# Kernel tuning notes

Hardware: AMD Instinct MI355X
Metric: run time of the kernel (lower is better)

## Reference

```python
import jax, jax.numpy as jnp
import numpy as np

B, SW, SE, D, H, FF = 8, 512, 128, 1024, 16, 4096
HD = D // H
EPS = 1e-12
SCALE = 1.0 / np.sqrt(HD).astype(np.float32)


def _split_heads(x):
    # [B, S, D] -> [B, H, S, HD]
    b, s, _ = x.shape
    return x.reshape(b, s, H, HD).transpose(0, 2, 1, 3)


def _layer_norm(x, g, b):
    m = jnp.mean(x, axis=-1, keepdims=True)
    v = jnp.mean(jnp.square(x - m), axis=-1, keepdims=True)
    return g * (x - m) / jnp.sqrt(v + EPS) + b


def setup_inputs() -> dict:
    key = jax.random.key(0)
    ks = iter(jax.random.split(key, 40))
    std = 0.02

    def w(i, o):
        return jax.random.normal(next(ks), (i, o), jnp.float32) * std

    inp = {
        "word_hidden_states": jax.random.normal(next(ks), (B, SW, D), jnp.float32),
        "entity_hidden_states": jax.random.normal(next(ks), (B, SE, D), jnp.float32),
        "word_attention_mask": jnp.zeros((B, SW), jnp.float32),
        "entity_attention_mask": jnp.zeros((B, SE), jnp.float32),
        # entity-aware self attention projections
        "Wq": w(D, D), "bq": jnp.zeros((D,), jnp.float32),
        "Ww2e": w(D, D), "bw2e": jnp.zeros((D,), jnp.float32),
        "We2w": w(D, D), "be2w": jnp.zeros((D,), jnp.float32),
        "We2e": w(D, D), "be2e": jnp.zeros((D,), jnp.float32),
        "Wk": w(D, D), "bk": jnp.zeros((D,), jnp.float32),
        "Wv": w(D, D), "bv": jnp.zeros((D,), jnp.float32),
        # BertSelfOutput
        "Wo": w(D, D), "bo": jnp.zeros((D,), jnp.float32),
        "ln1_g": jnp.ones((D,), jnp.float32), "ln1_b": jnp.zeros((D,), jnp.float32),
        # BertIntermediate / BertOutput
        "Wi": w(D, FF), "bi": jnp.zeros((FF,), jnp.float32),
        "Wout": w(FF, D), "bout": jnp.zeros((D,), jnp.float32),
        "ln2_g": jnp.ones((D,), jnp.float32), "ln2_b": jnp.zeros((D,), jnp.float32),
    }
    return inp


def _layer(wh, eh, wmask, emask, Wq, bq, Ww2e, bw2e, We2w, be2w, We2e, be2e,
           Wk, bk, Wv, bv, Wo, bo, ln1_g, ln1_b, Wi, bi, Wout, bout, ln2_g, ln2_b):
    sw = wh.shape[1]
    hidden = jnp.concatenate([wh, eh], axis=1)              # [B, S, D]
    mask = jnp.concatenate([wmask, emask], axis=-1)[:, None, None, :]  # additive

    q_w2w = _split_heads(wh @ Wq + bq)
    q_w2e = _split_heads(wh @ Ww2e + bw2e)
    q_e2w = _split_heads(eh @ We2w + be2w)
    q_e2e = _split_heads(eh @ We2e + be2e)
    k = _split_heads(hidden @ Wk + bk)                      # [B, H, S, HD]
    kw, ke = k[:, :, :sw, :], k[:, :, sw:, :]

    s_w2w = jnp.einsum("bhqd,bhkd->bhqk", q_w2w, kw)
    s_w2e = jnp.einsum("bhqd,bhkd->bhqk", q_w2e, ke)
    s_e2w = jnp.einsum("bhqd,bhkd->bhqk", q_e2w, kw)
    s_e2e = jnp.einsum("bhqd,bhkd->bhqk", q_e2e, ke)
    word_scores = jnp.concatenate([s_w2w, s_w2e], axis=3)
    ent_scores = jnp.concatenate([s_e2w, s_e2e], axis=3)
    scores = jnp.concatenate([word_scores, ent_scores], axis=2) * SCALE + mask
    probs = jax.nn.softmax(scores, axis=-1)

    v = _split_heads(hidden @ Wv + bv)
    ctx = jnp.einsum("bhqk,bhkd->bhqd", probs, v)
    ctx = ctx.transpose(0, 2, 1, 3).reshape(wh.shape[0], -1, D)  # [B, S, D]

    # BertSelfOutput: dense + residual + LN
    attn_out = _layer_norm(ctx @ Wo + bo + hidden, ln1_g, ln1_b)
    # BertIntermediate + BertOutput
    inter = jax.nn.gelu(attn_out @ Wi + bi, approximate=False)
    out = _layer_norm(inter @ Wout + bout + attn_out, ln2_g, ln2_b)
    return out[:, :sw, :], out[:, sw:, :]


def reference(word_hidden_states, entity_hidden_states, word_attention_mask,
              entity_attention_mask, Wq, bq, Ww2e, bw2e, We2w, be2w, We2e, be2e,
              Wk, bk, Wv, bv, Wo, bo, ln1_g, ln1_b, Wi, bi, Wout, bout,
              ln2_g, ln2_b):
    return _layer(word_hidden_states, entity_hidden_states, word_attention_mask,
                  entity_attention_mask, Wq, bq, Ww2e, bw2e, We2w, be2w, We2e,
                  be2e, Wk, bk, Wv, bv, Wo, bo, ln1_g, ln1_b, Wi, bi, Wout,
                  bout, ln2_g, ln2_b)
```

## Files before the change

kernel.cpp:

```cpp
#include <hip/hip_runtime.h>
#include <hip/hip_bf16.h>
#include <stdint.h>
#include <math.h>

#define DEV __device__ __forceinline__

using bf16 = __hip_bfloat16;
typedef __attribute__((ext_vector_type(8))) short bf16x8;
typedef __attribute__((ext_vector_type(4))) float f32x4;

static constexpr int NB  = 8;
static constexpr int NSW = 512;
static constexpr int NSE = 128;
static constexpr int ND  = 1024;
static constexpr int NH  = 16;
static constexpr int NFF = 4096;
static constexpr int NS  = NSW + NSE;
static constexpr int NHD = 64;

DEV f32x4 mfma16(bf16x8 a, bf16x8 b, f32x4 c){
  return __builtin_amdgcn_mfma_f32_16x16x32_bf16(a, b, c, 0, 0, 0);
}

DEV void gload16(const bf16* g, bf16* l){
  __builtin_amdgcn_global_load_lds((const __attribute__((address_space(1))) void*)g,
                                   (__attribute__((address_space(3))) void*)l,
                                   16, 0, 0);
}

DEV bf16 tobf(float f){ return __float2bfloat16(f); }

union PK4 { bf16 h[4]; short4 s; };

__global__ __launch_bounds__(256) void cast_word_k(const float* __restrict__ wh,
                                                   bf16* __restrict__ whb,
                                                   bf16* __restrict__ hid){
  long i = ((long)blockIdx.x*256 + threadIdx.x)*4;
  float4 v = *reinterpret_cast<const float4*>(wh + i);
  PK4 p; p.h[0]=tobf(v.x); p.h[1]=tobf(v.y); p.h[2]=tobf(v.z); p.h[3]=tobf(v.w);
  *reinterpret_cast<short4*>(whb + i) = p.s;
  long row = i >> 10; int c = (int)(i & 1023);
  int b = (int)(row >> 9), s = (int)(row & 511);
  *reinterpret_cast<short4*>(hid + ((long)(b*NS + s) << 10) + c) = p.s;
}

__global__ __launch_bounds__(256) void cast_ent_k(const float* __restrict__ eh,
                                                  bf16* __restrict__ ehb,
                                                  bf16* __restrict__ hid){
  long i = ((long)blockIdx.x*256 + threadIdx.x)*4;
  float4 v = *reinterpret_cast<const float4*>(eh + i);
  PK4 p; p.h[0]=tobf(v.x); p.h[1]=tobf(v.y); p.h[2]=tobf(v.z); p.h[3]=tobf(v.w);
  *reinterpret_cast<short4*>(ehb + i) = p.s;
  long row = i >> 10; int c = (int)(i & 1023);
  int b = (int)(row >> 7), s = (int)(row & 127);
  *reinterpret_cast<short4*>(hid + ((long)(b*NS + NSW + s) << 10) + c) = p.s;
}

struct TP7 { const float* src[7]; bf16* dst[7]; };

__global__ void transpose7_k(TP7 tp){
  __shared__ float tile[32][33];
  const float* in = tp.src[blockIdx.z];
  bf16* out = tp.dst[blockIdx.z];
  const int c0 = blockIdx.x*32, r0 = blockIdx.y*32;
  const int tx = threadIdx.x, ty = threadIdx.y;
  #pragma unroll
  for (int i=0;i<4;i++)
    tile[ty + i*8][tx] = in[(long)(r0 + ty + i*8)*1024 + c0 + tx];
  __syncthreads();
  #pragma unroll
  for (int i=0;i<4;i++){
    int rr = ty + i*8;
    out[(long)(c0 + rr)*1024 + r0 + tx] = tobf(tile[tx][rr]);
  }
}

__global__ void transpose_cast_k(const float* __restrict__ in, bf16* __restrict__ out,
                                 int R, int C){
  __shared__ float tile[32][33];
  const int c0 = blockIdx.x*32, r0 = blockIdx.y*32;
  const int tx = threadIdx.x, ty = threadIdx.y;
  #pragma unroll
  for (int i=0;i<4;i++)
    tile[ty + i*8][tx] = in[(long)(r0 + ty + i*8)*C + c0 + tx];
  __syncthreads();
  #pragma unroll
  for (int i=0;i<4;i++){
    int rr = ty + i*8;
    out[(long)(c0 + rr)*R + r0 + tx] = tobf(tile[tx][rr]);
  }
}

__global__ void bias_concat_k(const float* __restrict__ bq, const float* __restrict__ bw2e,
                              const float* __restrict__ be2w, const float* __restrict__ be2e,
                              const float* __restrict__ bk, const float* __restrict__ bv,
                              float* __restrict__ bQw, float* __restrict__ bQe,
                              float* __restrict__ bKV){
  int i = blockIdx.x*256 + threadIdx.x;
  bQw[i] = bq[i];   bQw[1024+i] = bw2e[i];
  bQe[i] = be2w[i]; bQe[1024+i] = be2e[i];
  bKV[i] = bk[i];   bKV[1024+i] = bv[i];
}

template<int EPI>
__global__ __launch_bounds__(256) void gemm_bt_k(const bf16* __restrict__ A,
                                                 const bf16* __restrict__ Bt,
                                                 const float* __restrict__ bias,
                                                 void* __restrict__ Cout,
                                                 void* __restrict__ Cout2,
                                                 int M, int N, int K){
  __shared__ __align__(16) bf16 As[128*64];
  __shared__ __align__(16) bf16 Bs[128*64];
  const int tid = threadIdx.x;

  const int nwg = gridDim.x*gridDim.y;
  const int orig = blockIdx.y*gridDim.x + blockIdx.x;
  const int qq = nwg >> 3, rr8 = nwg & 7;
  const int xcd = orig & 7, idx = orig >> 3;
  const int wg = (xcd < rr8 ? xcd*(qq+1) : rr8*(qq+1) + (xcd-rr8)*qq) + idx;
  const int m0 = (wg / gridDim.x)*128, n0 = (wg % gridDim.x)*128;

  const int Kc  = K / gridDim.z;
  const int kt0 = blockIdx.z * Kc;

  const int wid = tid>>6, lane = tid&63;
  const int wr = wid>>1, wc = wid&1;
  const int lr = lane&15, lg = lane>>4;

  const f32x4 zero = {0.f,0.f,0.f,0.f};
  f32x4 acc[4][4];
  #pragma unroll
  for (int m=0;m<4;m++)
    #pragma unroll
    for (int n=0;n<4;n++) acc[m][n] = zero;

  for (int kt=kt0; kt<kt0+Kc; kt+=64){
    #pragma unroll
    for (int i=0;i<4;i++){
      int idx2 = i*256 + tid;
      int row = idx2>>3, kc = idx2&7;
      gload16(A + (long)(m0+row)*K + kt + kc*8, As + idx2*8);
    }
    #pragma unroll
    for (int i=0;i<4;i++){
      int idx2 = i*256 + tid;
      int row = idx2>>3, kc = idx2&7;
      gload16(Bt + (long)(n0+row)*K + kt + kc*8, Bs + idx2*8);
    }
    __syncthreads();
    #pragma unroll
    for (int ks=0; ks<2; ks++){
      bf16x8 af[4], bg[4];
      #pragma unroll
      for (int m=0;m<4;m++)
        af[m] = *reinterpret_cast<const bf16x8*>(As + (wr*64 + m*16 + lr)*64 + ks*32 + lg*8);
      #pragma unroll
      for (int n=0;n<4;n++)
        bg[n] = *reinterpret_cast<const bf16x8*>(Bs + (wc*64 + n*16 + lr)*64 + ks*32 + lg*8);
      __builtin_amdgcn_s_setprio(1);
      #pragma unroll
      for (int m=0;m<4;m++)
        #pragma unroll
        for (int n=0;n<4;n++)
          acc[m][n] = mfma16(af[m], bg[n], acc[m][n]);
      __builtin_amdgcn_s_setprio(0);
    }
    __syncthreads();
  }

  #pragma unroll
  for (int m=0;m<4;m++){
    const int rbase = m0 + wr*64 + m*16 + lg*4;
    #pragma unroll
    for (int n=0;n<4;n++){
      const int col = n0 + wc*64 + n*16 + lr;
      const float bsv = (EPI == 5 && blockIdx.z != 0) ? 0.f : bias[col];
      #pragma unroll
      for (int r=0;r<4;r++){
        const int rw = rbase + r;
        float v = acc[m][n][r] + bsv;
        if constexpr (EPI == 0){
          ((bf16*)Cout)[(long)rw*N + col] = tobf(v);
        } else if constexpr (EPI == 3){
          float ge = 0.5f*v*(1.0f + erff(v*0.70710678118654752f));
          ((bf16*)Cout)[(long)rw*N + col] = tobf(ge);
        } else if constexpr (EPI == 4){
          if (col < 1024){
            ((bf16*)Cout)[(long)rw*2048 + col] = tobf(v);
          } else {
            int bb = rw / NS, ss = rw % NS, hh = (col-1024) >> 6, dd = (col-1024) & 63;
            ((bf16*)Cout2)[((long)((bb*NH + hh)*NHD + dd))*NS + ss] = tobf(v);
          }
        } else {
          float* dst = blockIdx.z == 0 ? (float*)Cout : (float*)Cout2;
          dst[(long)rw*N + col] = v;
        }
      }
    }
  }
}

__global__ __launch_bounds__(256) void attn_k(
    const bf16* __restrict__ Qw,
    const bf16* __restrict__ Qe,
    const bf16* __restrict__ KV,
    const bf16* __restrict__ Vt,
    const float* __restrict__ wm, const float* __restrict__ em,
    bf16* __restrict__ ctx){
  __shared__ __align__(16) bf16 Plds[4][2][16*40];
  __shared__ float mred[4][2][16];
  __shared__ float lred[4][2][16];
  __shared__ __align__(16) float accred[4][16][64];
  const int tid = threadIdx.x, wid = tid>>6, lane = tid&63;
  const int lr = lane&15, lg = lane>>4;
  const int w   = blockIdx.x;
  const int b   = w / (NH*20);
  const int rem = w % (NH*20);
  const int h   = rem / 20;
  const int q0  = (rem % 20)*32;

  const bf16* Qbase; long qrow0;
  if (q0 < NSW){ Qbase = Qw; qrow0 = (long)b*NSW + q0; }
  else         { Qbase = Qe; qrow0 = (long)b*NSE + (q0 - NSW); }

  bf16x8 qA[2][2], qB[2][2];
  #pragma unroll
  for (int m=0;m<2;m++)
    #pragma unroll
    for (int dc=0; dc<2; dc++){
      long o = (qrow0 + m*16 + lr)*2048 + h*NHD + dc*32 + lg*8;
      qA[m][dc] = *reinterpret_cast<const bf16x8*>(Qbase + o);
      qB[m][dc] = *reinterpret_cast<const bf16x8*>(Qbase + o + 1024);
    }

  const f32x4 zero = {0.f,0.f,0.f,0.f};
  f32x4 cacc[2][4];
  float mrow[2][4], lsum[2][4];
  #pragma unroll
  for (int m=0;m<2;m++){
    #pragma unroll
    for (int dt=0;dt<4;dt++) cacc[m][dt] = zero;
    #pragma unroll
    for (int r=0;r<4;r++){ mrow[m][r] = -1e30f; lsum[m][r] = 0.f; }
  }

  const bf16* Kbase = KV + (long)b*NS*2048 + h*NHD;
  const bf16* Vbase = Vt + (long)((b*NH + h)*NHD)*NS;

  for (int kt=wid*5; kt<wid*5+5; kt++){
    const int k0 = kt*32;
    const bool word = (k0 < NSW);

    bf16x8 kf[2][2], vf[4];
    #pragma unroll
    for (int sub=0;sub<2;sub++)
      #pragma unroll
      for (int dc=0;dc<2;dc++)
        kf[sub][dc] = *reinterpret_cast<const bf16x8*>(
            Kbase + (long)(k0 + sub*16 + lr)*2048 + dc*32 + lg*8);
    #pragma unroll
    for (int dt=0;dt<4;dt++)
      vf[dt] = *reinterpret_cast<const bf16x8*>(
          Vbase + (long)(dt*16 + lr)*NS + k0 + lg*8);

    float msk0, msk1;
    { int k = k0 + lr;
      msk0 = word ? wm[b*NSW + k]      : em[b*NSE + (k - NSW)];
      msk1 = word ? wm[b*NSW + k + 16] : em[b*NSE + (k + 16 - NSW)];
    }

    f32x4 sc[2][2];
    #pragma unroll
    for (int m=0;m<2;m++){ sc[m][0]=zero; sc[m][1]=zero; }
    __builtin_amdgcn_s_setprio(1);
    #pragma unroll
    for (int m=0;m<2;m++)
      #pragma unroll
      for (int sub=0;sub<2;sub++)
        #pragma unroll
        for (int dc=0;dc<2;dc++){
          const bf16x8 q = word ? qA[m][dc] : qB[m][dc];
          sc[m][sub] = mfma16(q, kf[sub][dc], sc[m][sub]);
        }
    __builtin_amdgcn_s_setprio(0);

    #pragma unroll
    for (int m=0;m<2;m++){
      bf16* pw = &Plds[wid][m][0];
      #pragma unroll
      for (int r=0;r<4;r++){
        float s0 = sc[m][0][r]*0.125f + msk0;
        float s1 = sc[m][1][r]*0.125f + msk1;
        float t = fmaxf(s0, s1);
        #pragma unroll
        for (int o=8;o;o>>=1) t = fmaxf(t, __shfl_xor(t, o, 16));
        float mn = fmaxf(mrow[m][r], t);
        float al = __expf(mrow[m][r] - mn);
        mrow[m][r] = mn;
        float p0 = __expf(s0 - mn), p1 = __expf(s1 - mn);
        float ps = p0 + p1;
        #pragma unroll
        for (int o=8;o;o>>=1) ps += __shfl_xor(ps, o, 16);
        lsum[m][r] = lsum[m][r]*al + ps;
        pw[(lg*4+r)*40 + lr]      = tobf(p0);
        pw[(lg*4+r)*40 + 16 + lr] = tobf(p1);
        #pragma unroll
        for (int dt=0;dt<4;dt++) cacc[m][dt][r] *= al;
      }
    }

    __builtin_amdgcn_s_setprio(1);
    #pragma unroll
    for (int m=0;m<2;m++){
      bf16x8 pa = *reinterpret_cast<const bf16x8*>(&Plds[wid][m][0] + lr*40 + lg*8);
      #pragma unroll
      for (int dt=0;dt<4;dt++)
        cacc[m][dt] = mfma16(pa, vf[dt], cacc[m][dt]);
    }
    __builtin_amdgcn_s_setprio(0);
  }

  #pragma unroll
  for (int m=0;m<2;m++)
    #pragma unroll
    for (int r=0;r<4;r++)
      if (lr == 0){
        mred[wid][m][lg*4+r] = mrow[m][r];
        lred[wid][m][lg*4+r] = lsum[m][r];
      }
  __syncthreads();

  float Lg[2][4], scl[2][4];
  #pragma unroll
  for (int m=0;m<2;m++)
    #pragma unroll
    for (int r=0;r<4;r++){
      const int row = lg*4 + r;
      float M0 = fmaxf(fmaxf(mred[0][m][row], mred[1][m][row]),
                       fmaxf(mred[2][m][row], mred[3][m][row]));
      float lt = 0.f;
      #pragma unroll
      for (int ww=0; ww<4; ww++)
        lt += lred[ww][m][row] * __expf(mred[ww][m][row] - M0);
      Lg[m][r]  = lt;
      scl[m][r] = __expf(mrow[m][r] - M0);
    }

  const long crow = (long)b*NS + q0;
  #pragma unroll
  for (int m=0;m<2;m++){
    #pragma unroll
    for (int dt=0;dt<4;dt++)
      #pragma unroll
      for (int r=0;r<4;r++)
        accred[wid][dt*4+r][lane] = cacc[m][dt][r] * scl[m][r];
    __syncthreads();
    { const int dt = wid;
      #pragma unroll
      for (int r=0;r<4;r++){
        float s = accred[0][dt*4+r][lane] + accred[1][dt*4+r][lane]
                + accred[2][dt*4+r][lane] + accred[3][dt*4+r][lane];
        s /= Lg[m][r];
        ctx[(crow + m*16 + lg*4 + r)*ND + h*NHD + dt*16 + lr] = tobf(s);
      }
    }
    __syncthreads();
  }
}

DEV void block_red2(float& s1, float& s2){
  __shared__ float red[8];
  #pragma unroll
  for (int o=32;o;o>>=1){ s1 += __shfl_down(s1,o); s2 += __shfl_down(s2,o); }
  int wid = threadIdx.x>>6, lane = threadIdx.x&63;
  if (lane==0){ red[wid]=s1; red[4+wid]=s2; }
  __syncthreads();
  s1 = red[0]+red[1]+red[2]+red[3];
  s2 = red[4]+red[5]+red[6]+red[7];
}

__global__ __launch_bounds__(256) void ln1_k(const float* __restrict__ ctxO,
    const float* __restrict__ ctxO1,
    const float* __restrict__ wh, const float* __restrict__ eh,
    const float* __restrict__ g, const float* __restrict__ be,
    float* __restrict__ outF, bf16* __restrict__ outB){
  const int row = blockIdx.x;
  const int b = row / NS, s = row % NS;
  const float* resid = (s < NSW) ? wh + ((long)(b*NSW + s))*ND
                                 : eh + ((long)(b*NSE + (s-NSW)))*ND;
  const int t = threadIdx.x;
  float4 xv = reinterpret_cast<const float4*>(ctxO + (long)row*ND)[t];
  float4 x1 = reinterpret_cast<const float4*>(ctxO1 + (long)row*ND)[t];
  float4 rv = reinterpret_cast<const float4*>(resid)[t];
  float4 x = make_float4(xv.x+x1.x+rv.x, xv.y+x1.y+rv.y, xv.z+x1.z+rv.z, xv.w+x1.w+rv.w);
  float s1 = x.x+x.y+x.z+x.w;
  float s2 = x.x*x.x + x.y*x.y + x.z*x.z + x.w*x.w;
  block_red2(s1, s2);
  float mean = s1 * (1.f/ND);
  float var  = s2 * (1.f/ND) - mean*mean;
  float rstd = rsqrtf(var + 1e-12f);
  float4 gv = reinterpret_cast<const float4*>(g)[t];
  float4 bv = reinterpret_cast<const float4*>(be)[t];
  float4 y = make_float4(gv.x*(x.x-mean)*rstd + bv.x,
                         gv.y*(x.y-mean)*rstd + bv.y,
                         gv.z*(x.z-mean)*rstd + bv.z,
                         gv.w*(x.w-mean)*rstd + bv.w);
  reinterpret_cast<float4*>(outF + (long)row*ND)[t] = y;
  PK4 p; p.h[0]=tobf(y.x); p.h[1]=tobf(y.y); p.h[2]=tobf(y.z); p.h[3]=tobf(y.w);
  reinterpret_cast<short4*>(outB + (long)row*ND)[t] = p.s;
}

__global__ __launch_bounds__(256) void ln2_k(const float* __restrict__ ffo,
    const float* __restrict__ ffo1,
    const float* __restrict__ attnF, const float* __restrict__ g,
    const float* __restrict__ be, float* __restrict__ out){
  const int row = blockIdx.x;
  const int b = row / NS, s = row % NS;
  const int t = threadIdx.x;
  float4 xv = reinterpret_cast<const float4*>(ffo + (long)row*ND)[t];
  float4 x1 = reinterpret_cast<const float4*>(ffo1 + (long)row*ND)[t];
  float4 rv = reinterpret_cast<const float4*>(attnF + (long)row*ND)[t];
  float4 x = make_float4(xv.x+x1.x+rv.x, xv.y+x1.y+rv.y, xv.z+x1.z+rv.z, xv.w+x1.w+rv.w);
  float s1 = x.x+x.y+x.z+x.w;
  float s2 = x.x*x.x + x.y*x.y + x.z*x.z + x.w*x.w;
  block_red2(s1, s2);
  float mean = s1 * (1.f/ND);
  float var  = s2 * (1.f/ND) - mean*mean;
  float rstd = rsqrtf(var + 1e-12f);
  float4 gv = reinterpret_cast<const float4*>(g)[t];
  float4 bv = reinterpret_cast<const float4*>(be)[t];
  float4 y = make_float4(gv.x*(x.x-mean)*rstd + bv.x,
                         gv.y*(x.y-mean)*rstd + bv.y,
                         gv.z*(x.z-mean)*rstd + bv.z,
                         gv.w*(x.w-mean)*rstd + bv.w);
  float* op = (s < NSW) ? out + ((long)(b*NSW+s))*ND
                        : out + (long)NB*NSW*ND + ((long)(b*NSE + (s-NSW)))*ND;
  reinterpret_cast<float4*>(op)[t] = y;
}

extern "C" void kernel_launch(void* const* d_in, const int* in_sizes, int n_in,
                              void* d_out, int out_size, void* d_ws, size_t ws_size,
                              hipStream_t stream){
  (void)in_sizes; (void)n_in; (void)out_size; (void)ws_size;
  const float* wh   = (const float*)d_in[0];
  const float* eh   = (const float*)d_in[1];
  const float* wm   = (const float*)d_in[2];
  const float* em   = (const float*)d_in[3];
  const float* Wq   = (const float*)d_in[4];   const float* bq   = (const float*)d_in[5];
  const float* Ww2e = (const float*)d_in[6];   const float* bw2e = (const float*)d_in[7];
  const float* We2w = (const float*)d_in[8];   const float* be2w = (const float*)d_in[9];
  const float* We2e = (const float*)d_in[10];  const float* be2e = (const float*)d_in[11];
  const float* Wk   = (const float*)d_in[12];  const float* bk   = (const float*)d_in[13];
  const float* Wv   = (const float*)d_in[14];  const float* bv   = (const float*)d_in[15];
  const float* Wo   = (const float*)d_in[16];  const float* bo   = (const float*)d_in[17];
  const float* g1   = (const float*)d_in[18];  const float* b1   = (const float*)d_in[19];
  const float* Wi   = (const float*)d_in[20];  const float* bi   = (const float*)d_in[21];
  const float* Wout = (const float*)d_in[22];  const float* bout = (const float*)d_in[23];
  const float* g2   = (const float*)d_in[24];  const float* b2   = (const float*)d_in[25];
  float* out = (float*)d_out;

  char* ws = (char*)d_ws;
  size_t off = 0;
  auto alloc = [&](size_t bytes)->char*{
    char* p = ws + off; off += (bytes + 255) & ~(size_t)255; return p;
  };

  bf16* hid   = (bf16*)alloc((size_t)NB*NS*ND*2);
  bf16* whb   = (bf16*)alloc((size_t)NB*NSW*ND*2);
  bf16* ehb   = (bf16*)alloc((size_t)NB*NSE*ND*2);
  float* part1 = (float*)hid;
  bf16* WqwT  = (bf16*)alloc((size_t)2048*ND*2);
  bf16* WqeT  = (bf16*)alloc((size_t)2048*ND*2);
  bf16* WkvT  = (bf16*)alloc((size_t)2048*ND*2);
  bf16* WoT   = (bf16*)alloc((size_t)ND*ND*2);
  bf16* WiT   = (bf16*)alloc((size_t)NFF*ND*2);
  bf16* WoutT = (bf16*)alloc((size_t)ND*NFF*2);
  float* bQw  = (float*)alloc(2048*4);
  float* bQe  = (float*)alloc(2048*4);
  float* bKV  = (float*)alloc(2048*4);

  char* u1 = alloc((size_t)52428800);
  bf16* Qwb = (bf16*)u1;
  bf16* Qeb = Qwb + (size_t)NB*NSW*2048;
  bf16* KVb = Qeb + (size_t)NB*NSE*2048;
  bf16* Vt  = KVb + (size_t)NB*NS*2048;
  bf16* inter = (bf16*)u1;
  bf16* attnB = (bf16*)(u1 + (size_t)41943040);

  bf16*  ctx   = (bf16*)alloc((size_t)NB*NS*ND*2);
  float* ctxO  = (float*)alloc((size_t)NB*NS*ND*4);
  float* ffo   = ctxO;
  float* attnF = (float*)alloc((size_t)NB*NS*ND*4);

  dim3 tb(32,8);
  cast_word_k<<<4096, 256, 0, stream>>>(wh, whb, hid);
  cast_ent_k <<<1024, 256, 0, stream>>>(eh, ehb, hid);

  TP7 tp;
  tp.src[0]=Wq;   tp.dst[0]=WqwT;
  tp.src[1]=Ww2e; tp.dst[1]=WqwT + (size_t)1024*1024;
  tp.src[2]=We2w; tp.dst[2]=WqeT;
  tp.src[3]=We2e; tp.dst[3]=WqeT + (size_t)1024*1024;
  tp.src[4]=Wk;   tp.dst[4]=WkvT;
  tp.src[5]=Wv;   tp.dst[5]=WkvT + (size_t)1024*1024;
  tp.src[6]=Wo;   tp.dst[6]=WoT;
  transpose7_k<<<dim3(32,32,7), tb, 0, stream>>>(tp);
  transpose_cast_k<<<dim3(128,32), tb, 0, stream>>>(Wi,   WiT,   ND, NFF);
  transpose_cast_k<<<dim3(32,128), tb, 0, stream>>>(Wout, WoutT, NFF, ND);
  bias_concat_k<<<4, 256, 0, stream>>>(bq, bw2e, be2w, be2e, bk, bv, bQw, bQe, bKV);

  gemm_bt_k<0><<<dim3(16,32), 256, 0, stream>>>(whb, WqwT, bQw, Qwb, nullptr, NB*NSW, 2048, ND);
  gemm_bt_k<0><<<dim3(16, 8), 256, 0, stream>>>(ehb, WqeT, bQe, Qeb, nullptr, NB*NSE, 2048, ND);
  gemm_bt_k<4><<<dim3(16,40), 256, 0, stream>>>(hid, WkvT, bKV, KVb, Vt,      NB*NS,  2048, ND);

  attn_k<<<2560, 256, 0, stream>>>(Qwb, Qeb, KVb, Vt, wm, em, ctx);

  gemm_bt_k<5><<<dim3(8,40,2),  256, 0, stream>>>(ctx,   WoT,   bo,   ctxO, part1, NB*NS, ND,  ND);
  ln1_k<<<5120, 256, 0, stream>>>(ctxO, part1, wh, eh, g1, b1, attnF, attnB);
  gemm_bt_k<3><<<dim3(32,40),   256, 0, stream>>>(attnB, WiT,   bi,   inter, nullptr, NB*NS, NFF, ND);
  gemm_bt_k<5><<<dim3(8,40,2),  256, 0, stream>>>(inter, WoutT, bout, ffo,  part1, NB*NS, ND,  NFF);
  ln2_k<<<5120, 256, 0, stream>>>(ffo, part1, attnF, g2, b2, out);
}
```

Measured before the change: 563.0 us.

## Replace GEMMs with 256-wide double-buffered core and merge projection launches

Replaces the generic 128x128 single-buffered GEMM with a 512-thread core using 256x256 (or 256x128 for split-K) tiles. The core double-buffers LDS, waits on vmcnt and overlaps the next K-slice loads with MFMA work. Its LDS layout is lane-ordered, so fragment reads are contiguous. The three Q/KV projection GEMMs become one launch that gathers word and entity rows straight from the concatenated hidden buffer, which removes the separate whb/ehb bf16 copies. The aim is to raise data reuse and hide global load latency, at the cost of heavy LDS use that limits occupancy to one block per CU and fewer blocks per launch.

```diff
diff --git a/kernel.cpp b/kernel.cpp
--- a/kernel.cpp
+++ b/kernel.cpp
@@ -33,24 +33,20 @@
 union PK4 { bf16 h[4]; short4 s; };
 
 __global__ __launch_bounds__(256) void cast_word_k(const float* __restrict__ wh,
-                                                   bf16* __restrict__ whb,
                                                    bf16* __restrict__ hid){
   long i = ((long)blockIdx.x*256 + threadIdx.x)*4;
   float4 v = *reinterpret_cast<const float4*>(wh + i);
   PK4 p; p.h[0]=tobf(v.x); p.h[1]=tobf(v.y); p.h[2]=tobf(v.z); p.h[3]=tobf(v.w);
-  *reinterpret_cast<short4*>(whb + i) = p.s;
   long row = i >> 10; int c = (int)(i & 1023);
   int b = (int)(row >> 9), s = (int)(row & 511);
   *reinterpret_cast<short4*>(hid + ((long)(b*NS + s) << 10) + c) = p.s;
 }
 
 __global__ __launch_bounds__(256) void cast_ent_k(const float* __restrict__ eh,
-                                                  bf16* __restrict__ ehb,
                                                   bf16* __restrict__ hid){
   long i = ((long)blockIdx.x*256 + threadIdx.x)*4;
   float4 v = *reinterpret_cast<const float4*>(eh + i);
   PK4 p; p.h[0]=tobf(v.x); p.h[1]=tobf(v.y); p.h[2]=tobf(v.z); p.h[3]=tobf(v.w);
-  *reinterpret_cast<short4*>(ehb + i) = p.s;
   long row = i >> 10; int c = (int)(i & 1023);
   int b = (int)(row >> 7), s = (int)(row & 127);
   *reinterpret_cast<short4*>(hid + ((long)(b*NS + NSW + s) << 10) + c) = p.s;
@@ -102,109 +98,232 @@
   bKV[i] = bk[i];   bKV[1024+i] = bv[i];
 }
 
-template<int EPI>
-__global__ __launch_bounds__(256) void gemm_bt_k(const bf16* __restrict__ A,
-                                                 const bf16* __restrict__ Bt,
-                                                 const float* __restrict__ bias,
-                                                 void* __restrict__ Cout,
-                                                 void* __restrict__ Cout2,
-                                                 int M, int N, int K){
-  __shared__ __align__(16) bf16 As[128*64];
-  __shared__ __align__(16) bf16 Bs[128*64];
-  const int tid = threadIdx.x;
-
-  const int nwg = gridDim.x*gridDim.y;
-  const int orig = blockIdx.y*gridDim.x + blockIdx.x;
-  const int qq = nwg >> 3, rr8 = nwg & 7;
-  const int xcd = orig & 7, idx = orig >> 3;
-  const int wg = (xcd < rr8 ? xcd*(qq+1) : rr8*(qq+1) + (xcd-rr8)*qq) + idx;
-  const int m0 = (wg / gridDim.x)*128, n0 = (wg % gridDim.x)*128;
-
-  const int Kc  = K / gridDim.z;
-  const int kt0 = blockIdx.z * Kc;
-
-  const int wid = tid>>6, lane = tid&63;
-  const int wr = wid>>1, wc = wid&1;
-  const int lr = lane&15, lg = lane>>4;
-
-  const f32x4 zero = {0.f,0.f,0.f,0.f};
-  f32x4 acc[4][4];
-  #pragma unroll
-  for (int m=0;m<4;m++)
-    #pragma unroll
-    for (int n=0;n<4;n++) acc[m][n] = zero;
-
-  for (int kt=kt0; kt<kt0+Kc; kt+=64){
-    #pragma unroll
-    for (int i=0;i<4;i++){
-      int idx2 = i*256 + tid;
-      int row = idx2>>3, kc = idx2&7;
-      gload16(A + (long)(m0+row)*K + kt + kc*8, As + idx2*8);
-    }
-    #pragma unroll
-    for (int i=0;i<4;i++){
-      int idx2 = i*256 + tid;
-      int row = idx2>>3, kc = idx2&7;
-      gload16(Bt + (long)(n0+row)*K + kt + kc*8, Bs + idx2*8);
-    }
-    __syncthreads();
-    #pragma unroll
-    for (int ks=0; ks<2; ks++){
-      bf16x8 af[4], bg[4];
-      #pragma unroll
-      for (int m=0;m<4;m++)
-        af[m] = *reinterpret_cast<const bf16x8*>(As + (wr*64 + m*16 + lr)*64 + ks*32 + lg*8);
-      #pragma unroll
-      for (int n=0;n<4;n++)
-        bg[n] = *reinterpret_cast<const bf16x8*>(Bs + (wc*64 + n*16 + lr)*64 + ks*32 + lg*8);
+template<int NF>
+DEV void stA(bf16* reg, const bf16* a0, const bf16* a1, int koff, int tid){
+  gload16(a0 + koff, reg + tid*8);
+  gload16(a1 + koff, reg + (512 + tid)*8);
+}
+template<int NF>
+DEV void stB(bf16* reg, const bf16* b0, const bf16* b1, int koff, int tid){
+  gload16(b0 + koff, reg + tid*8);
+  if constexpr (NF == 4) gload16(b1 + koff, reg + (512 + tid)*8);
+}
+
+template<int NF>
+DEV void g256_core(const bf16* a0, const bf16* a1,
+                   const bf16* b0, const bf16* b1,
+                   int NT, bf16* lds, f32x4 (&acc)[8][NF],
+                   int tid, int wr, int wc, int lane){
+  constexpr int AKH  = 8192;
+  constexpr int BKH  = NF*2048;
+  constexpr int BUFE = 2*AKH + 2*BKH;
+  auto Areg = [&](int buf,int kh){ return lds + buf*BUFE + kh*AKH; };
+  auto Breg = [&](int buf,int kh){ return lds + buf*BUFE + 2*AKH + kh*BKH; };
+  auto gate = [&](bool last){
+    if (last){
+      asm volatile("s_waitcnt vmcnt(0)" ::: "memory");
+    } else if constexpr (NF == 4){
+      asm volatile("s_waitcnt vmcnt(4)" ::: "memory");
+    } else {
+      asm volatile("s_waitcnt vmcnt(3)" ::: "memory");
+    }
+    __builtin_amdgcn_sched_barrier(0);
+    asm volatile("s_barrier" ::: "memory");
+    __builtin_amdgcn_sched_barrier(0);
+  };
+  stA<NF>(Areg(0,0), a0, a1, 0,  tid);
+  stB<NF>(Breg(0,0), b0, b1, 0,  tid);
+  stA<NF>(Areg(0,1), a0, a1, 32, tid);
+  stB<NF>(Breg(0,1), b0, b1, 32, tid);
+  int kt = 0;
+  for (int t=0; t<NT; ++t){
+    const int c = t & 1;
+    const bool more = (t+1 < NT);
+    const int kn = kt + 64;
+    #pragma unroll
+    for (int ks=0; ks<2; ++ks){
+      gate(!more && ks==1);
+      if (more) stA<NF>(Areg(c^1, ks), a0, a1, kn + ks*32, tid);
+      const bf16* Ar = Areg(c, ks);
+      const bf16* Br = Breg(c, ks);
+      bf16x8 bfr[NF], afr[4];
+      #pragma unroll
+      for (int nf=0; nf<NF; ++nf)
+        bfr[nf] = *reinterpret_cast<const bf16x8*>(Br + (((wc*NF+nf)<<6) + lane)*8);
+      #pragma unroll
+      for (int m=0; m<4; ++m)
+        afr[m] = *reinterpret_cast<const bf16x8*>(Ar + (((wr*8+m)<<6) + lane)*8);
       __builtin_amdgcn_s_setprio(1);
       #pragma unroll
-      for (int m=0;m<4;m++)
+      for (int m=0; m<4; ++m)
         #pragma unroll
-        for (int n=0;n<4;n++)
-          acc[m][n] = mfma16(af[m], bg[n], acc[m][n]);
+        for (int nf=0; nf<NF; ++nf)
+          acc[m][nf] = mfma16(afr[m], bfr[nf], acc[m][nf]);
       __builtin_amdgcn_s_setprio(0);
-    }
-    __syncthreads();
-  }
-
-  #pragma unroll
-  for (int m=0;m<4;m++){
-    const int rbase = m0 + wr*64 + m*16 + lg*4;
-    #pragma unroll
-    for (int n=0;n<4;n++){
-      const int col = n0 + wc*64 + n*16 + lr;
-      const float bsv = (EPI == 5 && blockIdx.z != 0) ? 0.f : bias[col];
+      if (more) stB<NF>(Breg(c^1, ks), b0, b1, kn + ks*32, tid);
+      #pragma unroll
+      for (int m=0; m<4; ++m)
+        afr[m] = *reinterpret_cast<const bf16x8*>(Ar + (((wr*8+4+m)<<6) + lane)*8);
+      __builtin_amdgcn_s_setprio(1);
+      #pragma unroll
+      for (int m=0; m<4; ++m)
+        #pragma unroll
+        for (int nf=0; nf<NF; ++nf)
+          acc[4+m][nf] = mfma16(afr[m], bfr[nf], acc[4+m][nf]);
+      __builtin_amdgcn_s_setprio(0);
+    }
+    kt = kn;
+  }
+}
+
+__global__ __launch_bounds__(512, 2) void proj_k(const bf16* __restrict__ hid,
+    const bf16* __restrict__ WqwT, const bf16* __restrict__ WqeT,
+    const bf16* __restrict__ WkvT,
+    const float* __restrict__ bQw, const float* __restrict__ bQe,
+    const float* __restrict__ bKV,
+    bf16* __restrict__ Qwb, bf16* __restrict__ Qeb,
+    bf16* __restrict__ KVb, bf16* __restrict__ Vt){
+  __shared__ __align__(16) bf16 lds[2*(2*8192 + 2*8192)];
+  const int tid = threadIdx.x, wid = tid>>6, lane = tid&63;
+  const int wr = wid>>2, wc = wid&3, lr = lane&15, lg = lane>>4;
+  int wg = blockIdx.x;
+  { int xcd = wg & 7, idx = wg >> 3; wg = xcd*40 + idx; }
+  const bool isKV = (wg >= 160);
+  const int loc = isKV ? wg - 160 : wg;
+  const int m0 = (loc >> 3)*256, n0 = (loc & 7)*256;
+  const bool word = (m0 < 4096);
+
+  const int la = lane & 15, ksub = (lane>>4)*8;
+  auto hidrow = [&](int r)->long{
+    if (isKV) return r;
+    if (word) return (long)((r>>9)*640 + (r&511));
+    int r2 = r - 4096; return (long)((r2>>7)*640 + 512 + (r2&127));
+  };
+  const bf16* a0 = hid + hidrow(m0 + wid*16 + la)*1024 + ksub;
+  const bf16* a1 = hid + hidrow(m0 + (wid+8)*16 + la)*1024 + ksub;
+  const bf16* Bt = isKV ? WkvT : (word ? WqwT : WqeT);
+  const bf16* b0 = Bt + (long)(n0 + wid*16 + la)*1024 + ksub;
+  const bf16* b1 = Bt + (long)(n0 + (wid+8)*16 + la)*1024 + ksub;
+
+  f32x4 acc[8][4];
+  #pragma unroll
+  for (int m=0;m<8;m++)
+    #pragma unroll
+    for (int n=0;n<4;n++) acc[m][n] = (f32x4){0.f,0.f,0.f,0.f};
+
+  g256_core<4>(a0, a1, b0, b1, 16, lds, acc, tid, wr, wc, lane);
+
+  const float* bias = isKV ? bKV : (word ? bQw : bQe);
+  #pragma unroll
+  for (int m=0;m<8;m++){
+    const int rbase = m0 + wr*128 + m*16 + lg*4;
+    #pragma unroll
+    for (int nf=0;nf<4;nf++){
+      const int col = n0 + wc*64 + nf*16 + lr;
+      const float bsv = bias[col];
       #pragma unroll
       for (int r=0;r<4;r++){
         const int rw = rbase + r;
-        float v = acc[m][n][r] + bsv;
-        if constexpr (EPI == 0){
-          ((bf16*)Cout)[(long)rw*N + col] = tobf(v);
-        } else if constexpr (EPI == 3){
-          float ge = 0.5f*v*(1.0f + erff(v*0.70710678118654752f));
-          ((bf16*)Cout)[(long)rw*N + col] = tobf(ge);
-        } else if constexpr (EPI == 4){
+        const float v = acc[m][nf][r] + bsv;
+        if (!isKV){
+          if (word) Qwb[(long)rw*2048 + col] = tobf(v);
+          else      Qeb[(long)(rw-4096)*2048 + col] = tobf(v);
+        } else {
           if (col < 1024){
-            ((bf16*)Cout)[(long)rw*2048 + col] = tobf(v);
+            KVb[(long)rw*2048 + col] = tobf(v);
           } else {
-            int bb = rw / NS, ss = rw % NS, hh = (col-1024) >> 6, dd = (col-1024) & 63;
-            ((bf16*)Cout2)[((long)((bb*NH + hh)*NHD + dd))*NS + ss] = tobf(v);
+            int b = rw / NS, s = rw % NS, hh = (col-1024)>>6, dd = (col-1024)&63;
+            Vt[((long)((b*NH + hh)*NHD + dd))*NS + s] = tobf(v);
           }
-        } else {
-          float* dst = blockIdx.z == 0 ? (float*)Cout : (float*)Cout2;
-          dst[(long)rw*N + col] = v;
         }
       }
     }
   }
 }
 
+__global__ __launch_bounds__(512, 2) void ffn1_k(const bf16* __restrict__ A,
+    const bf16* __restrict__ Bt, const float* __restrict__ bias,
+    bf16* __restrict__ out){
+  __shared__ __align__(16) bf16 lds[2*(2*8192 + 2*8192)];
+  const int tid = threadIdx.x, wid = tid>>6, lane = tid&63;
+  const int wr = wid>>2, wc = wid&3, lr = lane&15, lg = lane>>4;
+  int wg = blockIdx.x;
+  { int xcd = wg & 7, idx = wg >> 3; wg = xcd*40 + idx; }
+  const int m0 = (wg >> 4)*256, n0 = (wg & 15)*256;
+
+  const int la = lane & 15, ksub = (lane>>4)*8;
+  const bf16* a0 = A + (long)(m0 + wid*16 + la)*1024 + ksub;
+  const bf16* a1 = A + (long)(m0 + (wid+8)*16 + la)*1024 + ksub;
+  const bf16* b0 = Bt + (long)(n0 + wid*16 + la)*1024 + ksub;
+  const bf16* b1 = Bt + (long)(n0 + (wid+8)*16 + la)*1024 + ksub;
+
+  f32x4 acc[8][4];
+  #pragma unroll
+  for (int m=0;m<8;m++)
+    #pragma unroll
+    for (int n=0;n<4;n++) acc[m][n] = (f32x4){0.f,0.f,0.f,0.f};
+
+  g256_core<4>(a0, a1, b0, b1, 16, lds, acc, tid, wr, wc, lane);
+
+  #pragma unroll
+  for (int m=0;m<8;m++){
+    const int rbase = m0 + wr*128 + m*16 + lg*4;
+    #pragma unroll
+    for (int nf=0;nf<4;nf++){
+      const int col = n0 + wc*64 + nf*16 + lr;
+      const float bsv = bias[col];
+      #pragma unroll
+      for (int r=0;r<4;r++){
+        float v = acc[m][nf][r] + bsv;
+        float ge = 0.5f*v*(1.0f + erff(v*0.70710678118654752f));
+        out[(long)(rbase+r)*NFF + col] = tobf(ge);
+      }
+    }
+  }
+}
+
+__global__ __launch_bounds__(512, 2) void ws_k(const bf16* __restrict__ A, int lda,
+    const bf16* __restrict__ Bt, const float* __restrict__ bias,
+    float* __restrict__ out0, float* __restrict__ out1, int Kc){
+  __shared__ __align__(16) bf16 lds[2*(2*8192 + 2*4096)];
+  const int tid = threadIdx.x, wid = tid>>6, lane = tid&63;
+  const int wr = wid>>2, wc = wid&3, lr = lane&15, lg = lane>>4;
+  int wg = blockIdx.x;
+  { int xcd = wg & 7, idx = wg >> 3; wg = xcd*20 + idx; }
+  const int m0 = (wg >> 3)*256, n0 = (wg & 7)*128;
+  const int kt0 = blockIdx.z * Kc;
+
+  const int la = lane & 15, ksub = (lane>>4)*8;
+  const bf16* a0 = A + (long)(m0 + wid*16 + la)*lda + kt0 + ksub;
+  const bf16* a1 = A + (long)(m0 + (wid+8)*16 + la)*lda + kt0 + ksub;
+  const bf16* b0 = Bt + (long)(n0 + wid*16 + la)*lda + kt0 + ksub;
+
+  f32x4 acc[8][2];
+  #pragma unroll
+  for (int m=0;m<8;m++)
+    #pragma unroll
+    for (int n=0;n<2;n++) acc[m][n] = (f32x4){0.f,0.f,0.f,0.f};
+
+  g256_core<2>(a0, a1, b0, b0, Kc/64, lds, acc, tid, wr, wc, lane);
+
+  float* out = blockIdx.z ? out1 : out0;
+  #pragma unroll
+  for (int m=0;m<8;m++){
+    const int rbase = m0 + wr*128 + m*16 + lg*4;
+    #pragma unroll
+    for (int nf=0;nf<2;nf++){
+      const int col = n0 + wc*32 + nf*16 + lr;
+      const float bsv = blockIdx.z ? 0.f : bias[col];
+      #pragma unroll
+      for (int r=0;r<4;r++)
+        out[(long)(rbase+r)*1024 + col] = acc[m][nf][r] + bsv;
+    }
+  }
+}
+
 __global__ __launch_bounds__(256) void attn_k(
-    const bf16* __restrict__ Qw,
-    const bf16* __restrict__ Qe,
-    const bf16* __restrict__ KV,
-    const bf16* __restrict__ Vt,
+    const bf16* __restrict__ Qw, const bf16* __restrict__ Qe,
+    const bf16* __restrict__ KV, const bf16* __restrict__ Vt,
     const float* __restrict__ wm, const float* __restrict__ em,
     bf16* __restrict__ ctx){
   __shared__ __align__(16) bf16 Plds[4][2][16*40];
@@ -466,12 +585,10 @@
   };
 
   bf16* hid   = (bf16*)alloc((size_t)NB*NS*ND*2);
-  bf16* whb   = (bf16*)alloc((size_t)NB*NSW*ND*2);
-  bf16* ehb   = (bf16*)alloc((size_t)NB*NSE*ND*2);
-  float* part1 = (float*)hid;
   bf16* WqwT  = (bf16*)alloc((size_t)2048*ND*2);
   bf16* WqeT  = (bf16*)alloc((size_t)2048*ND*2);
   bf16* WkvT  = (bf16*)alloc((size_t)2048*ND*2);
+  float* part1 = (float*)hid;
   bf16* WoT   = (bf16*)alloc((size_t)ND*ND*2);
   bf16* WiT   = (bf16*)alloc((size_t)NFF*ND*2);
   bf16* WoutT = (bf16*)alloc((size_t)ND*NFF*2);
@@ -493,8 +610,8 @@
   float* attnF = (float*)alloc((size_t)NB*NS*ND*4);
 
   dim3 tb(32,8);
-  cast_word_k<<<4096, 256, 0, stream>>>(wh, whb, hid);
-  cast_ent_k <<<1024, 256, 0, stream>>>(eh, ehb, hid);
+  cast_word_k<<<4096, 256, 0, stream>>>(wh, hid);
+  cast_ent_k <<<1024, 256, 0, stream>>>(eh, hid);
 
   TP7 tp;
   tp.src[0]=Wq;   tp.dst[0]=WqwT;
@@ -509,15 +626,14 @@
   transpose_cast_k<<<dim3(32,128), tb, 0, stream>>>(Wout, WoutT, NFF, ND);
   bias_concat_k<<<4, 256, 0, stream>>>(bq, bw2e, be2w, be2e, bk, bv, bQw, bQe, bKV);
 
-  gemm_bt_k<0><<<dim3(16,32), 256, 0, stream>>>(whb, WqwT, bQw, Qwb, nullptr, NB*NSW, 2048, ND);
-  gemm_bt_k<0><<<dim3(16, 8), 256, 0, stream>>>(ehb, WqeT, bQe, Qeb, nullptr, NB*NSE, 2048, ND);
-  gemm_bt_k<4><<<dim3(16,40), 256, 0, stream>>>(hid, WkvT, bKV, KVb, Vt,      NB*NS,  2048, ND);
+  proj_k<<<320, 512, 0, stream>>>(hid, WqwT, WqeT, WkvT, bQw, bQe, bKV,
+                                  Qwb, Qeb, KVb, Vt);
 
   attn_k<<<2560, 256, 0, stream>>>(Qwb, Qeb, KVb, Vt, wm, em, ctx);
 
-  gemm_bt_k<5><<<dim3(8,40,2),  256, 0, stream>>>(ctx,   WoT,   bo,   ctxO, part1, NB*NS, ND,  ND);
+  ws_k<<<dim3(160,1,2), 512, 0, stream>>>(ctx, 1024, WoT, bo, ctxO, part1, 512);
   ln1_k<<<5120, 256, 0, stream>>>(ctxO, part1, wh, eh, g1, b1, attnF, attnB);
-  gemm_bt_k<3><<<dim3(32,40),   256, 0, stream>>>(attnB, WiT,   bi,   inter, nullptr, NB*NS, NFF, ND);
-  gemm_bt_k<5><<<dim3(8,40,2),  256, 0, stream>>>(inter, WoutT, bout, ffo,  part1, NB*NS, ND,  NFF);
+  ffn1_k<<<320, 512, 0, stream>>>(attnB, WiT, bi, inter);
+  ws_k<<<dim3(160,1,2), 512, 0, stream>>>(inter, 4096, WoutT, bout, ffo, part1, 2048);
   ln2_k<<<5120, 256, 0, stream>>>(ffo, part1, attnF, g2, b2, out);
 }
```

Measured after the change: 633.1 us. +12.4%, slower.
